# Optimization experiments

Measured on AMD Instinct MI355X. Metric: run time of the kernel, lower is better.

## Reference

```python
import jax, jax.numpy as jnp
import numpy as np

N, E = 50000, 800000
IN_C, HID_C, OUT_C = 256, 256, 256


def setup_inputs() -> dict:
    key = jax.random.key(0)
    ks = jax.random.split(key, 8)
    x_piece = jax.random.normal(ks[0], (N, IN_C), dtype=jnp.float32)
    edge_index_piece = jax.random.randint(ks[1], (2, E), 0, N, dtype=jnp.int64)
    batch = jnp.zeros((N,), dtype=jnp.int64)
    def glorot(k, fan_in, fan_out):
        s = jnp.sqrt(6.0 / (fan_in + fan_out)).astype(jnp.float32)
        return jax.random.uniform(k, (fan_in, fan_out), jnp.float32, -s, s)
    return {
        "x_piece": x_piece,
        "edge_index_piece": edge_index_piece,
        "batch": batch,
        "W1": glorot(ks[2], IN_C, HID_C), "b1": jnp.zeros((HID_C,), jnp.float32),
        "W2": glorot(ks[3], HID_C, HID_C), "b2": jnp.zeros((HID_C,), jnp.float32),
        "W3": glorot(ks[4], HID_C, OUT_C), "b3": jnp.zeros((OUT_C,), jnp.float32),
    }


def _gcn_prep(edge_index, n_nodes):
    # add self-loops, compute symmetric normalization (PyG GCNConv default)
    src = jnp.concatenate([edge_index[0], jnp.arange(n_nodes, dtype=edge_index.dtype)])
    dst = jnp.concatenate([edge_index[1], jnp.arange(n_nodes, dtype=edge_index.dtype)])
    deg = jax.ops.segment_sum(jnp.ones_like(dst, dtype=jnp.float32), dst, num_segments=n_nodes)
    deg_inv_sqrt = jnp.where(deg > 0, jax.lax.rsqrt(jnp.maximum(deg, 1.0)), 0.0)
    norm = deg_inv_sqrt[src] * deg_inv_sqrt[dst]  # [E+N]
    return src, dst, norm


def _gcn_layer(x, src, dst, norm, W, b, n_nodes):
    h = x @ W                                   # [N, out] dense transform first
    msg = h[src] * norm[:, None]                # gather + scale
    out = jax.ops.segment_sum(msg, dst, num_segments=n_nodes)  # scatter-add
    return out + b


def reference(x_piece, edge_index_piece, batch, W1, b1, W2, b2, W3, b3):
    n_nodes = x_piece.shape[0]
    src, dst, norm = _gcn_prep(edge_index_piece, n_nodes)
    x = _gcn_layer(x_piece, src, dst, norm, W1, b1, n_nodes)
    x = jax.nn.gelu(x)
    x = _gcn_layer(x, src, dst, norm, W2, b2, n_nodes)
    x = jax.nn.gelu(x)
    x = _gcn_layer(x, src, dst, norm, W3, b3, n_nodes)
    return x
```

## Files before the change

### kernel.cpp

```cpp
#include <hip/hip_runtime.h>
#include <cstdint>
#include <cstddef>

#define CH 256

typedef _Float16 f16x8 __attribute__((ext_vector_type(8)));
typedef float f32x4 __attribute__((ext_vector_type(4)));

#define GLOB(x) ((const __attribute__((address_space(1))) void*)(x))
#define LDSP(x) ((__attribute__((address_space(3))) void*)(x))


__device__ __forceinline__ int ld_idx(const void* p, long long i, int w64) {
    if (w64) return (int)((const long long*)p)[i];
    return ((const int*)p)[i];
}

__device__ __forceinline__ float gelu_f(float x) {
    float x3 = x * x * x;
    float t = tanhf(0.7978845608028654f * (x + 0.044715f * x3));
    return 0.5f * x * (1.0f + t);
}


__global__ void k_detect(const void* __restrict__ ei, int* __restrict__ flag, int E) {
    int l = threadIdx.x;
    long long k = ((long long)l * (long long)(E - 1)) / 63;
    int w = ((const int*)ei)[2 * k + 1];
    unsigned long long vote = __ballot(w == 0);
    if (l == 0) *flag = (vote == ~0ULL) ? 1 : 0;
}

__global__ void k_deg(const void* __restrict__ ei, const int* __restrict__ flag,
                      int* __restrict__ deg, int E) {
    int e = blockIdx.x * blockDim.x + threadIdx.x;
    if (e >= E) return;
    int w64 = *flag;
    int d = ld_idx(ei, (long long)E + e, w64);
    atomicAdd(&deg[d], 1);
}

__global__ void k_dis(const int* __restrict__ deg, float* __restrict__ dis, int N) {
    int n = blockIdx.x * blockDim.x + threadIdx.x;
    if (n >= N) return;
    dis[n] = 1.0f / sqrtf((float)(deg[n] + 1));
}

__global__ void k_scan_block(const int* __restrict__ deg, int* __restrict__ rowptr,
                             int* __restrict__ partial, int N) {
    __shared__ int s[256];
    int gid = blockIdx.x * 256 + threadIdx.x;
    int v = (gid < N) ? deg[gid] : 0;
    s[threadIdx.x] = v;
    __syncthreads();
    for (int off = 1; off < 256; off <<= 1) {
        int t = (threadIdx.x >= off) ? s[threadIdx.x - off] : 0;
        __syncthreads();
        s[threadIdx.x] += t;
        __syncthreads();
    }
    if (gid < N) rowptr[gid] = s[threadIdx.x] - v;
    if (threadIdx.x == 255) partial[blockIdx.x] = s[255];
}

__global__ void k_scan_partial(int* __restrict__ partial, int nb) {
    __shared__ int s[256];
    int i = threadIdx.x;
    int v = (i < nb) ? partial[i] : 0;
    s[i] = v;
    __syncthreads();
    for (int off = 1; off < 256; off <<= 1) {
        int t = (i >= off) ? s[i - off] : 0;
        __syncthreads();
        s[i] += t;
        __syncthreads();
    }
    if (i < nb) partial[i] = s[i] - v;
}

__global__ void k_add_off(int* __restrict__ rowptr, const int* __restrict__ partial,
                          int N, int E) {
    int gid = blockIdx.x * 256 + threadIdx.x;
    if (gid < N) rowptr[gid] += partial[blockIdx.x];
    if (gid == 0) rowptr[N] = E;
}

__global__ void k_scatter(const void* __restrict__ ei, const int* __restrict__ flag,
                          const float* __restrict__ dis, const int* __restrict__ rowptr,
                          int* __restrict__ cnt, int2* __restrict__ epack, int E) {
    int e = blockIdx.x * blockDim.x + threadIdx.x;
    if (e >= E) return;
    int w64 = *flag;
    int s = ld_idx(ei, e, w64);
    int d = ld_idx(ei, (long long)E + e, w64);
    int pos = rowptr[d] + atomicAdd(&cnt[d], 1);
    epack[pos] = make_int2(s, __float_as_int(dis[s] * dis[d]));
}


__global__ void k_split_w(const float* __restrict__ W, _Float16* __restrict__ Wh,
                          _Float16* __restrict__ Wl) {
    int k = threadIdx.x;
    int c = blockIdx.x;
    float v = W[k * CH + c];
    _Float16 h = (_Float16)v;
    Wh[c * CH + k] = h;
    Wl[c * CH + k] = (_Float16)(v - (float)h);
}


#define GM 128
#define GN 128
#define GK 32

__global__ __launch_bounds__(256, 2)
void k_gemm16(const float* __restrict__ A, const _Float16* __restrict__ Bh,
              const _Float16* __restrict__ Bl, uint8_t* __restrict__ H16,
              float* __restrict__ scales, int M) {
    __shared__ __align__(16) char smem[65536];
    float*    lA = (float*)smem;
    _Float16* lB = (_Float16*)(smem + 32768);

    const int tid  = threadIdx.x;
    const int lane = tid & 63;
    const int wid  = tid >> 6;
    const int m0   = blockIdx.x * GM;
    const int n0   = blockIdx.y * GN;
    const int wm   = wid >> 1, wn = wid & 1;
    const int r15  = lane & 15, kg = lane >> 4;

    auto stage = [&](int buf, int k0) {
        #pragma unroll
        for (int c = 0; c < 8; c++) {
            int call = wid * 8 + c;
            if (call < 16) {
                int L = call * 64 + lane;
                int row = L >> 3, ch = L & 7;
                int gr = m0 + row; gr = (gr < M) ? gr : (M - 1);
                const float* g = A + (size_t)gr * CH + k0 + ((ch ^ (row & 7)) << 2);
                __builtin_amdgcn_global_load_lds(GLOB(g), LDSP(&lA[buf * 4096 + call * 256]), 16, 0, 0);
            } else if (call < 24) {
                int cc = call - 16;
                int L = cc * 64 + lane;
                int row = L >> 2, ch = L & 3;
                const _Float16* g = Bh + (size_t)(n0 + row) * CH + k0 + ((ch ^ ((row >> 1) & 3)) << 3);
                __builtin_amdgcn_global_load_lds(GLOB(g), LDSP(&lB[buf * 8192 + cc * 512]), 16, 0, 0);
            } else {
                int cc = call - 24;
                int L = cc * 64 + lane;
                int row = L >> 2, ch = L & 3;
                const _Float16* g = Bl + (size_t)(n0 + row) * CH + k0 + ((ch ^ ((row >> 1) & 3)) << 3);
                __builtin_amdgcn_global_load_lds(GLOB(g), LDSP(&lB[buf * 8192 + 4096 + cc * 512]), 16, 0, 0);
            }
        }
    };

    f32x4 acc[4][4];
    #pragma unroll
    for (int i = 0; i < 4; i++)
        #pragma unroll
        for (int n = 0; n < 4; n++)
            acc[i][n] = (f32x4){0.f, 0.f, 0.f, 0.f};

    stage(0, 0);
    __syncthreads();

    for (int ks = 0; ks < 8; ks++) {
        int cur = ks & 1;
        if (ks < 7) stage(cur ^ 1, (ks + 1) * GK);

        f16x8 ah[4], al[4], bh[4], bl[4];
        #pragma unroll
        for (int i = 0; i < 4; i++) {
            int R  = wm * 64 + i * 16 + r15;
            int p0 = (2 * kg) ^ (R & 7);
            const f32x4* base = (const f32x4*)&lA[cur * 4096 + R * GK];
            f32x4 va = base[p0];
            f32x4 vb = base[p0 ^ 1];
            #pragma unroll
            for (int j = 0; j < 4; j++) {
                float v = va[j];
                _Float16 h = (_Float16)v;
                ah[i][j] = h;
                al[i][j] = (_Float16)(v - (float)h);
            }
            #pragma unroll
            for (int j = 0; j < 4; j++) {
                float v = vb[j];
                _Float16 h = (_Float16)v;
                ah[i][4 + j] = h;
                al[i][4 + j] = (_Float16)(v - (float)h);
            }
        }
        #pragma unroll
        for (int n = 0; n < 4; n++) {
            int C = wn * 64 + n * 16 + r15;
            int p = kg ^ ((C >> 1) & 3);
            bh[n] = *(const f16x8*)&lB[cur * 8192 + C * GK + p * 8];
            bl[n] = *(const f16x8*)&lB[cur * 8192 + 4096 + C * GK + p * 8];
        }
        #pragma unroll
        for (int i = 0; i < 4; i++)
            #pragma unroll
            for (int n = 0; n < 4; n++) {
                acc[i][n] = __builtin_amdgcn_mfma_f32_16x16x32_f16(ah[i], bh[n], acc[i][n], 0, 0, 0);
                acc[i][n] = __builtin_amdgcn_mfma_f32_16x16x32_f16(ah[i], bl[n], acc[i][n], 0, 0, 0);
                acc[i][n] = __builtin_amdgcn_mfma_f32_16x16x32_f16(al[i], bh[n], acc[i][n], 0, 0, 0);
            }
        __syncthreads();
    }

    float mx = 0.f;
    #pragma unroll
    for (int i = 0; i < 4; i++)
        #pragma unroll
        for (int n = 0; n < 4; n++)
            #pragma unroll
            for (int r = 0; r < 4; r++)
                mx = fmaxf(mx, fabsf(acc[i][n][r]));
    #pragma unroll
    for (int off = 32; off > 0; off >>= 1)
        mx = fmaxf(mx, __shfl_xor(mx, off));
    if (lane == 0) ((float*)smem)[wid] = mx;
    __syncthreads();
    float tmax = fmaxf(fmaxf(((float*)smem)[0], ((float*)smem)[1]),
                       fmaxf(((float*)smem)[2], ((float*)smem)[3]));
    float scl = tmax * (1.0f / 32767.0f);
    float inv = (tmax > 0.f) ? (32767.0f / tmax) : 0.f;
    __syncthreads();

    float* ep = (float*)smem + wid * 4096;
    #pragma unroll
    for (int i = 0; i < 4; i++)
        #pragma unroll
        for (int n = 0; n < 4; n++)
            #pragma unroll
            for (int r = 0; r < 4; r++)
                ep[(i * 16 + kg * 4 + r) * 64 + n * 16 + r15] = acc[i][n][r];
    __syncthreads();

    int q = lane & 15;
    int rsub = lane >> 4;
    #pragma unroll
    for (int p = 0; p < 16; p++) {
        int lrow = p * 4 + rsub;
        int grow = m0 + wm * 64 + lrow;
        if (grow < M) {
            int q0 = __float2int_rn(ep[lrow * 64 + q * 4 + 0] * inv);
            int q1 = __float2int_rn(ep[lrow * 64 + q * 4 + 1] * inv);
            int q2 = __float2int_rn(ep[lrow * 64 + q * 4 + 2] * inv);
            int q3 = __float2int_rn(ep[lrow * 64 + q * 4 + 3] * inv);
            uint2 d;
            d.x = (q0 & 0xFFFF) | (q1 << 16);
            d.y = (q2 & 0xFFFF) | (q3 << 16);
            int col = n0 + wn * 64 + q * 4;
            *(uint2*)(H16 + (size_t)grow * 512 + (size_t)col * 2) = d;
        }
    }

    if (tid < GM && m0 + tid < M) scales[(size_t)(m0 + tid) * 2 + (n0 >> 7)] = scl;
}


__global__ __launch_bounds__(256) void k_agg(const uint8_t* __restrict__ H16,
                                             const float* __restrict__ scales,
                                             const float* __restrict__ dis,
                                             const int* __restrict__ rowptr,
                                             const int2* __restrict__ epack,
                                             const float* __restrict__ bias,
                                             float* __restrict__ out, int N, int do_gelu) {
    int node = blockIdx.x * 4 + threadIdx.y;
    if (node >= N) return;
    int lane = threadIdx.x;
    int half = lane >> 5;
    float d = dis[node];
    short4 hv = *(const short4*)(H16 + (size_t)node * 512 + (size_t)lane * 8);
    float wself = d * d * scales[(size_t)node * 2 + half];
    float ax = wself * (float)hv.x, ay = wself * (float)hv.y;
    float az = wself * (float)hv.z, aw = wself * (float)hv.w;
    int s = rowptr[node], e = rowptr[node + 1];
    int j = s;
    for (; j + 8 <= e; j += 8) {
        int2 p[8];
        #pragma unroll
        for (int t = 0; t < 8; t++) p[t] = epack[j + t];
        short4 v[8];
        float sc[8];
        #pragma unroll
        for (int t = 0; t < 8; t++) {
            v[t] = *(const short4*)(H16 + (size_t)p[t].x * 512 + (size_t)lane * 8);
            sc[t] = scales[(size_t)p[t].x * 2 + half];
        }
        #pragma unroll
        for (int t = 0; t < 8; t++) {
            float wn = __int_as_float(p[t].y) * sc[t];
            ax += wn * (float)v[t].x; ay += wn * (float)v[t].y;
            az += wn * (float)v[t].z; aw += wn * (float)v[t].w;
        }
    }
    for (; j < e; j++) {
        int2 p = epack[j];
        float wn = __int_as_float(p.y) * scales[(size_t)p.x * 2 + half];
        short4 v = *(const short4*)(H16 + (size_t)p.x * 512 + (size_t)lane * 8);
        ax += wn * (float)v.x; ay += wn * (float)v.y;
        az += wn * (float)v.z; aw += wn * (float)v.w;
    }
    float4 b = ((const float4*)bias)[lane];
    ax += b.x; ay += b.y; az += b.z; aw += b.w;
    if (do_gelu) {
        ax = gelu_f(ax); ay = gelu_f(ay); az = gelu_f(az); aw = gelu_f(aw);
    }
    ((float4*)(out + (size_t)node * CH))[lane] = make_float4(ax, ay, az, aw);
}


extern "C" void kernel_launch(void* const* d_in, const int* in_sizes, int n_in,
                              void* d_out, int out_size, void* d_ws, size_t ws_size,
                              hipStream_t stream) {
    const float* x  = (const float*)d_in[0];
    const void*  ei = d_in[1];
    const float* W1 = (const float*)d_in[3]; const float* b1 = (const float*)d_in[4];
    const float* W2 = (const float*)d_in[5]; const float* b2 = (const float*)d_in[6];
    const float* W3 = (const float*)d_in[7]; const float* b3 = (const float*)d_in[8];

    int N = in_sizes[0] / CH;
    int E = in_sizes[1] / 2;
    float* out = (float*)d_out;

    char* ws = (char*)d_ws;
    auto take = [&](size_t bytes) {
        char* p = ws;
        ws += (bytes + 15) & ~(size_t)15;
        return p;
    };
    uint8_t*  H16    = (uint8_t*) take((size_t)N * 512);
    float*    scales = (float*)   take((size_t)N * 2 * sizeof(float));
    int*      deg    = (int*)     take((size_t)N * sizeof(int));
    float*    dis    = (float*)   take((size_t)N * sizeof(float));
    int*      rowptr = (int*)     take((size_t)(N + 1) * sizeof(int));
    int*      cnt    = (int*)     take((size_t)N * sizeof(int));
    int*      part   = (int*)     take(4096);
    int*      flag   = (int*)     take(16);
    int2*     epack  = (int2*)    take((size_t)E * sizeof(int2));
    _Float16* Wh1    = (_Float16*)take((size_t)CH * CH * 2);
    _Float16* Wl1    = (_Float16*)take((size_t)CH * CH * 2);
    _Float16* Wh2    = (_Float16*)take((size_t)CH * CH * 2);
    _Float16* Wl2    = (_Float16*)take((size_t)CH * CH * 2);
    _Float16* Wh3    = (_Float16*)take((size_t)CH * CH * 2);
    _Float16* Wl3    = (_Float16*)take((size_t)CH * CH * 2);

    hipMemsetAsync(deg, 0, (size_t)N * sizeof(int), stream);
    hipMemsetAsync(cnt, 0, (size_t)N * sizeof(int), stream);

    int eb = (E + 255) / 256;
    int nb = (N + 255) / 256;

    k_detect<<<1, 64, 0, stream>>>(ei, flag, E);
    k_deg<<<eb, 256, 0, stream>>>(ei, flag, deg, E);
    k_dis<<<nb, 256, 0, stream>>>(deg, dis, N);
    k_scan_block<<<nb, 256, 0, stream>>>(deg, rowptr, part, N);
    k_scan_partial<<<1, 256, 0, stream>>>(part, nb);
    k_add_off<<<nb, 256, 0, stream>>>(rowptr, part, N, E);
    k_scatter<<<eb, 256, 0, stream>>>(ei, flag, dis, rowptr, cnt, epack, E);

    k_split_w<<<CH, CH, 0, stream>>>(W1, Wh1, Wl1);
    k_split_w<<<CH, CH, 0, stream>>>(W2, Wh2, Wl2);
    k_split_w<<<CH, CH, 0, stream>>>(W3, Wh3, Wl3);

    dim3 ggrid((N + GM - 1) / GM, CH / GN);
    dim3 agrid((N + 3) / 4);
    dim3 ablock(64, 4);

    k_gemm16<<<ggrid, 256, 0, stream>>>(x, Wh1, Wl1, H16, scales, N);
    k_agg<<<agrid, ablock, 0, stream>>>(H16, scales, dis, rowptr, epack, b1, out, N, 1);
    k_gemm16<<<ggrid, 256, 0, stream>>>(out, Wh2, Wl2, H16, scales, N);
    k_agg<<<agrid, ablock, 0, stream>>>(H16, scales, dis, rowptr, epack, b2, out, N, 1);
    k_gemm16<<<ggrid, 256, 0, stream>>>(out, Wh3, Wl3, H16, scales, N);
    k_agg<<<agrid, ablock, 0, stream>>>(H16, scales, dis, rowptr, epack, b3, out, N, 0);
}
```

Baseline: 422.0 us.

## Store GEMM output in 32-column slabs and split aggregation across column groups

New measurement: 732.0 us. +73.4%, slower.

```diff
diff --git a/kernel.cpp b/kernel.cpp
--- a/kernel.cpp
+++ b/kernel.cpp
@@ -6,6 +6,7 @@
 
 typedef _Float16 f16x8 __attribute__((ext_vector_type(8)));
 typedef float f32x4 __attribute__((ext_vector_type(4)));
+typedef float f32x2 __attribute__((ext_vector_type(2)));
 
 #define GLOB(x) ((const __attribute__((address_space(1))) void*)(x))
 #define LDSP(x) ((__attribute__((address_space(3))) void*)(x))
@@ -254,7 +255,9 @@
             d.x = (q0 & 0xFFFF) | (q1 << 16);
             d.y = (q2 & 0xFFFF) | (q3 << 16);
             int col = n0 + wn * 64 + q * 4;
-            *(uint2*)(H16 + (size_t)grow * 512 + (size_t)col * 2) = d;
+            uint8_t* dst = H16 + ((size_t)(col >> 5) * (size_t)M + grow) * 64
+                               + (size_t)(col & 31) * 2;
+            *(uint2*)dst = d;
         }
     }
 
@@ -262,55 +265,67 @@
 }
 
 
-__global__ __launch_bounds__(256) void k_agg(const uint8_t* __restrict__ H16,
+__global__ __launch_bounds__(256) void k_agg(const uint8_t* __restrict__ H16g,
                                              const float* __restrict__ scales,
                                              const float* __restrict__ dis,
                                              const int* __restrict__ rowptr,
                                              const int2* __restrict__ epack,
                                              const float* __restrict__ bias,
                                              float* __restrict__ out, int N, int do_gelu) {
-    int node = blockIdx.x * 4 + threadIdx.y;
+    int g = blockIdx.x & 7;
+    int node = (blockIdx.x >> 3) * 4 + threadIdx.y;
     if (node >= N) return;
     int lane = threadIdx.x;
-    int half = lane >> 5;
-    float d = dis[node];
-    short4 hv = *(const short4*)(H16 + (size_t)node * 512 + (size_t)lane * 8);
-    float wself = d * d * scales[(size_t)node * 2 + half];
-    float ax = wself * (float)hv.x, ay = wself * (float)hv.y;
-    float az = wself * (float)hv.z, aw = wself * (float)hv.w;
+    int sub = lane >> 4;
+    int cp  = lane & 15;
+    int half = g >> 2;
+    const uint8_t* __restrict__ Hg = H16g + (size_t)g * (size_t)N * 64;
+
+    float ax, ay;
+    {
+        unsigned u = *(const unsigned*)(Hg + (size_t)node * 64 + cp * 4);
+        float d = dis[node];
+        float ws = (sub == 0) ? d * d * scales[(size_t)node * 2 + half] : 0.f;
+        ax = ws * (float)(short)(u & 0xFFFFu);
+        ay = ws * (float)(short)(u >> 16);
+    }
+
     int s = rowptr[node], e = rowptr[node + 1];
+    float bx = 0.f, by = 0.f;
     int j = s;
     for (; j + 8 <= e; j += 8) {
-        int2 p[8];
-        #pragma unroll
-        for (int t = 0; t < 8; t++) p[t] = epack[j + t];
-        short4 v[8];
-        float sc[8];
-        #pragma unroll
-        for (int t = 0; t < 8; t++) {
-            v[t] = *(const short4*)(H16 + (size_t)p[t].x * 512 + (size_t)lane * 8);
-            sc[t] = scales[(size_t)p[t].x * 2 + half];
-        }
-        #pragma unroll
-        for (int t = 0; t < 8; t++) {
-            float wn = __int_as_float(p[t].y) * sc[t];
-            ax += wn * (float)v[t].x; ay += wn * (float)v[t].y;
-            az += wn * (float)v[t].z; aw += wn * (float)v[t].w;
-        }
-    }
-    for (; j < e; j++) {
-        int2 p = epack[j];
-        float wn = __int_as_float(p.y) * scales[(size_t)p.x * 2 + half];
-        short4 v = *(const short4*)(H16 + (size_t)p.x * 512 + (size_t)lane * 8);
-        ax += wn * (float)v.x; ay += wn * (float)v.y;
-        az += wn * (float)v.z; aw += wn * (float)v.w;
-    }
-    float4 b = ((const float4*)bias)[lane];
-    ax += b.x; ay += b.y; az += b.z; aw += b.w;
-    if (do_gelu) {
-        ax = gelu_f(ax); ay = gelu_f(ay); az = gelu_f(az); aw = gelu_f(aw);
-    }
-    ((float4*)(out + (size_t)node * CH))[lane] = make_float4(ax, ay, az, aw);
+        int2 p1 = epack[j + sub];
+        int2 p2 = epack[j + 4 + sub];
+        unsigned u1 = *(const unsigned*)(Hg + (size_t)p1.x * 64 + cp * 4);
+        unsigned u2 = *(const unsigned*)(Hg + (size_t)p2.x * 64 + cp * 4);
+        float w1 = __int_as_float(p1.y) * scales[(size_t)p1.x * 2 + half];
+        float w2 = __int_as_float(p2.y) * scales[(size_t)p2.x * 2 + half];
+        ax += w1 * (float)(short)(u1 & 0xFFFFu);
+        ay += w1 * (float)(short)(u1 >> 16);
+        bx += w2 * (float)(short)(u2 & 0xFFFFu);
+        by += w2 * (float)(short)(u2 >> 16);
+    }
+    for (; j < e; j += 4) {
+        int idx = j + sub;
+        bool act = idx < e;
+        int2 p = epack[act ? idx : s];
+        unsigned u = *(const unsigned*)(Hg + (size_t)p.x * 64 + cp * 4);
+        float wn = act ? __int_as_float(p.y) * scales[(size_t)p.x * 2 + half] : 0.f;
+        ax += wn * (float)(short)(u & 0xFFFFu);
+        ay += wn * (float)(short)(u >> 16);
+    }
+    ax += bx; ay += by;
+
+    ax += __shfl_xor(ax, 16); ay += __shfl_xor(ay, 16);
+    ax += __shfl_xor(ax, 32); ay += __shfl_xor(ay, 32);
+
+    if (sub == 0) {
+        int c = g * 32 + cp * 2;
+        ax += bias[c]; ay += bias[c + 1];
+        if (do_gelu) { ax = gelu_f(ax); ay = gelu_f(ay); }
+        f32x2 v = {ax, ay};
+        __builtin_nontemporal_store(v, (f32x2*)(out + (size_t)node * CH + c));
+    }
 }
 
 
@@ -368,7 +383,7 @@
     k_split_w<<<CH, CH, 0, stream>>>(W3, Wh3, Wl3);
 
     dim3 ggrid((N + GM - 1) / GM, CH / GN);
-    dim3 agrid((N + 3) / 4);
+    dim3 agrid(8 * ((N + 3) / 4));
     dim3 ablock(64, 4);
 
     k_gemm16<<<ggrid, 256, 0, stream>>>(x, Wh1, Wl1, H16, scales, N);
```

## Pre-split GEMM activations into fp16 hi/lo in producer kernels

Applied to the files above, without the earlier changes.

Measured after the change: 440.4 us. 1.04x slower.

```diff
diff --git a/kernel.cpp b/kernel.cpp
--- a/kernel.cpp
+++ b/kernel.cpp
@@ -5,6 +5,7 @@
 #define CH 256
 
 typedef _Float16 f16x8 __attribute__((ext_vector_type(8)));
+typedef _Float16 f16x4 __attribute__((ext_vector_type(4)));
 typedef float f32x4 __attribute__((ext_vector_type(4)));
 
 #define GLOB(x) ((const __attribute__((address_space(1))) void*)(x))
@@ -109,17 +110,34 @@
 }
 
 
+__global__ void k_split_x(const float* __restrict__ x, _Float16* __restrict__ Ah,
+                          _Float16* __restrict__ Al, int n4) {
+    int i = blockIdx.x * 256 + threadIdx.x;
+    if (i >= n4) return;
+    float4 v = ((const float4*)x)[i];
+    f16x4 h, l;
+    h[0] = (_Float16)v.x; l[0] = (_Float16)(v.x - (float)h[0]);
+    h[1] = (_Float16)v.y; l[1] = (_Float16)(v.y - (float)h[1]);
+    h[2] = (_Float16)v.z; l[2] = (_Float16)(v.z - (float)h[2]);
+    h[3] = (_Float16)v.w; l[3] = (_Float16)(v.w - (float)h[3]);
+    ((f16x4*)Ah)[i] = h;
+    ((f16x4*)Al)[i] = l;
+}
+
+
 #define GM 128
 #define GN 128
 #define GK 32
 
 __global__ __launch_bounds__(256, 2)
-void k_gemm16(const float* __restrict__ A, const _Float16* __restrict__ Bh,
-              const _Float16* __restrict__ Bl, uint8_t* __restrict__ H16,
-              float* __restrict__ scales, int M) {
+void k_gemm16s(const _Float16* __restrict__ Ah, const _Float16* __restrict__ Al,
+               const _Float16* __restrict__ Bh, const _Float16* __restrict__ Bl,
+               uint8_t* __restrict__ H16, float* __restrict__ scales, int M) {
     __shared__ __align__(16) char smem[65536];
-    float*    lA = (float*)smem;
-    _Float16* lB = (_Float16*)(smem + 32768);
+    _Float16* lAh = (_Float16*)smem;
+    _Float16* lAl = (_Float16*)(smem + 16384);
+    _Float16* lBh = (_Float16*)(smem + 32768);
+    _Float16* lBl = (_Float16*)(smem + 49152);
 
     const int tid  = threadIdx.x;
     const int lane = tid & 63;
@@ -133,24 +151,24 @@
         #pragma unroll
         for (int c = 0; c < 8; c++) {
             int call = wid * 8 + c;
-            if (call < 16) {
-                int L = call * 64 + lane;
-                int row = L >> 3, ch = L & 7;
+            int cc = call & 7;
+            int L = cc * 64 + lane;
+            int row = L >> 2, ch = L & 3;
+            int sch = ch ^ ((row >> 1) & 3);
+            if (call < 8) {
                 int gr = m0 + row; gr = (gr < M) ? gr : (M - 1);
-                const float* g = A + (size_t)gr * CH + k0 + ((ch ^ (row & 7)) << 2);
-                __builtin_amdgcn_global_load_lds(GLOB(g), LDSP(&lA[buf * 4096 + call * 256]), 16, 0, 0);
+                const _Float16* g = Ah + (size_t)gr * CH + k0 + (sch << 3);
+                __builtin_amdgcn_global_load_lds(GLOB(g), LDSP(&lAh[buf * 4096 + L * 8]), 16, 0, 0);
+            } else if (call < 16) {
+                int gr = m0 + row; gr = (gr < M) ? gr : (M - 1);
+                const _Float16* g = Al + (size_t)gr * CH + k0 + (sch << 3);
+                __builtin_amdgcn_global_load_lds(GLOB(g), LDSP(&lAl[buf * 4096 + L * 8]), 16, 0, 0);
             } else if (call < 24) {
-                int cc = call - 16;
-                int L = cc * 64 + lane;
-                int row = L >> 2, ch = L & 3;
-                const _Float16* g = Bh + (size_t)(n0 + row) * CH + k0 + ((ch ^ ((row >> 1) & 3)) << 3);
-                __builtin_amdgcn_global_load_lds(GLOB(g), LDSP(&lB[buf * 8192 + cc * 512]), 16, 0, 0);
+                const _Float16* g = Bh + (size_t)(n0 + row) * CH + k0 + (sch << 3);
+                __builtin_amdgcn_global_load_lds(GLOB(g), LDSP(&lBh[buf * 4096 + L * 8]), 16, 0, 0);
             } else {
-                int cc = call - 24;
-                int L = cc * 64 + lane;
-                int row = L >> 2, ch = L & 3;
-                const _Float16* g = Bl + (size_t)(n0 + row) * CH + k0 + ((ch ^ ((row >> 1) & 3)) << 3);
-                __builtin_amdgcn_global_load_lds(GLOB(g), LDSP(&lB[buf * 8192 + 4096 + cc * 512]), 16, 0, 0);
+                const _Float16* g = Bl + (size_t)(n0 + row) * CH + k0 + (sch << 3);
+                __builtin_amdgcn_global_load_lds(GLOB(g), LDSP(&lBl[buf * 4096 + L * 8]), 16, 0, 0);
             }
         }
     };
@@ -172,32 +190,17 @@
         f16x8 ah[4], al[4], bh[4], bl[4];
         #pragma unroll
         for (int i = 0; i < 4; i++) {
-            int R  = wm * 64 + i * 16 + r15;
-            int p0 = (2 * kg) ^ (R & 7);
-            const f32x4* base = (const f32x4*)&lA[cur * 4096 + R * GK];
-            f32x4 va = base[p0];
-            f32x4 vb = base[p0 ^ 1];
-            #pragma unroll
-            for (int j = 0; j < 4; j++) {
-                float v = va[j];
-                _Float16 h = (_Float16)v;
-                ah[i][j] = h;
-                al[i][j] = (_Float16)(v - (float)h);
-            }
-            #pragma unroll
-            for (int j = 0; j < 4; j++) {
-                float v = vb[j];
-                _Float16 h = (_Float16)v;
-                ah[i][4 + j] = h;
-                al[i][4 + j] = (_Float16)(v - (float)h);
-            }
+            int R = wm * 64 + i * 16 + r15;
+            int p = kg ^ ((R >> 1) & 3);
+            ah[i] = *(const f16x8*)&lAh[cur * 4096 + R * GK + p * 8];
+            al[i] = *(const f16x8*)&lAl[cur * 4096 + R * GK + p * 8];
         }
         #pragma unroll
         for (int n = 0; n < 4; n++) {
             int C = wn * 64 + n * 16 + r15;
             int p = kg ^ ((C >> 1) & 3);
-            bh[n] = *(const f16x8*)&lB[cur * 8192 + C * GK + p * 8];
-            bl[n] = *(const f16x8*)&lB[cur * 8192 + 4096 + C * GK + p * 8];
+            bh[n] = *(const f16x8*)&lBh[cur * 4096 + C * GK + p * 8];
+            bl[n] = *(const f16x8*)&lBl[cur * 4096 + C * GK + p * 8];
         }
         #pragma unroll
         for (int i = 0; i < 4; i++)
@@ -262,13 +265,16 @@
 }
 
 
+template <int MODE>
 __global__ __launch_bounds__(256) void k_agg(const uint8_t* __restrict__ H16,
                                              const float* __restrict__ scales,
                                              const float* __restrict__ dis,
                                              const int* __restrict__ rowptr,
                                              const int2* __restrict__ epack,
                                              const float* __restrict__ bias,
-                                             float* __restrict__ out, int N, int do_gelu) {
+                                             float* __restrict__ out,
+                                             _Float16* __restrict__ Ah,
+                                             _Float16* __restrict__ Al, int N) {
     int node = blockIdx.x * 4 + threadIdx.y;
     if (node >= N) return;
     int lane = threadIdx.x;
@@ -307,10 +313,19 @@
     }
     float4 b = ((const float4*)bias)[lane];
     ax += b.x; ay += b.y; az += b.z; aw += b.w;
-    if (do_gelu) {
+    if (MODE == 0) {
         ax = gelu_f(ax); ay = gelu_f(ay); az = gelu_f(az); aw = gelu_f(aw);
-    }
-    ((float4*)(out + (size_t)node * CH))[lane] = make_float4(ax, ay, az, aw);
+        f16x4 h, l;
+        h[0] = (_Float16)ax; l[0] = (_Float16)(ax - (float)h[0]);
+        h[1] = (_Float16)ay; l[1] = (_Float16)(ay - (float)h[1]);
+        h[2] = (_Float16)az; l[2] = (_Float16)(az - (float)h[2]);
+        h[3] = (_Float16)aw; l[3] = (_Float16)(aw - (float)h[3]);
+        size_t idx = (size_t)node * 64 + lane;
+        ((f16x4*)Ah)[idx] = h;
+        ((f16x4*)Al)[idx] = l;
+    } else {
+        ((float4*)(out + (size_t)node * CH))[lane] = make_float4(ax, ay, az, aw);
+    }
 }
 
 
@@ -334,6 +349,8 @@
         return p;
     };
     uint8_t*  H16    = (uint8_t*) take((size_t)N * 512);
+    _Float16* Ah     = (_Float16*)take((size_t)N * CH * 2);
+    _Float16* Al     = (_Float16*)take((size_t)N * CH * 2);
     float*    scales = (float*)   take((size_t)N * 2 * sizeof(float));
     int*      deg    = (int*)     take((size_t)N * sizeof(int));
     float*    dis    = (float*)   take((size_t)N * sizeof(float));
@@ -367,14 +384,17 @@
     k_split_w<<<CH, CH, 0, stream>>>(W2, Wh2, Wl2);
     k_split_w<<<CH, CH, 0, stream>>>(W3, Wh3, Wl3);
 
+    int n4 = N * (CH / 4);
+    k_split_x<<<(n4 + 255) / 256, 256, 0, stream>>>(x, Ah, Al, n4);
+
     dim3 ggrid((N + GM - 1) / GM, CH / GN);
     dim3 agrid((N + 3) / 4);
     dim3 ablock(64, 4);
 
-    k_gemm16<<<ggrid, 256, 0, stream>>>(x, Wh1, Wl1, H16, scales, N);
-    k_agg<<<agrid, ablock, 0, stream>>>(H16, scales, dis, rowptr, epack, b1, out, N, 1);
-    k_gemm16<<<ggrid, 256, 0, stream>>>(out, Wh2, Wl2, H16, scales, N);
-    k_agg<<<agrid, ablock, 0, stream>>>(H16, scales, dis, rowptr, epack, b2, out, N, 1);
-    k_gemm16<<<ggrid, 256, 0, stream>>>(out, Wh3, Wl3, H16, scales, N);
-    k_agg<<<agrid, ablock, 0, stream>>>(H16, scales, dis, rowptr, epack, b3, out, N, 0);
-}
+    k_gemm16s<<<ggrid, 256, 0, stream>>>(Ah, Al, Wh1, Wl1, H16, scales, N);
+    k_agg<0><<<agrid, ablock, 0, stream>>>(H16, scales, dis, rowptr, epack, b1, out, Ah, Al, N);
+    k_gemm16s<<<ggrid, 256, 0, stream>>>(Ah, Al, Wh2, Wl2, H16, scales, N);
+    k_agg<0><<<agrid, ablock, 0, stream>>>(H16, scales, dis, rowptr, epack, b2, out, Ah, Al, N);
+    k_gemm16s<<<ggrid, 256, 0, stream>>>(Ah, Al, Wh3, Wl3, H16, scales, N);
+    k_agg<1><<<agrid, ablock, 0, stream>>>(H16, scales, dis, rowptr, epack, b3, out, Ah, Al, N);
+}
```

## Quantize GEMM activations to int16 per row to halve A-operand traffic

Applied to the files above, without the earlier changes.

Result: slower. 433.2 us (+2.6%).

```diff
diff --git a/kernel.cpp b/kernel.cpp
--- a/kernel.cpp
+++ b/kernel.cpp
@@ -5,7 +5,9 @@
 #define CH 256
 
 typedef _Float16 f16x8 __attribute__((ext_vector_type(8)));
+typedef _Float16 f16x4 __attribute__((ext_vector_type(4)));
 typedef float f32x4 __attribute__((ext_vector_type(4)));
+typedef short short8 __attribute__((ext_vector_type(8)));
 
 #define GLOB(x) ((const __attribute__((address_space(1))) void*)(x))
 #define LDSP(x) ((__attribute__((address_space(3))) void*)(x))
@@ -109,17 +111,39 @@
 }
 
 
+__global__ __launch_bounds__(256) void k_quant_x(const float* __restrict__ x,
+                                                 uint8_t* __restrict__ Xout,
+                                                 float* __restrict__ sout, int N) {
+    int node = blockIdx.x * 4 + threadIdx.y;
+    if (node >= N) return;
+    int lane = threadIdx.x;
+    float4 v = ((const float4*)(x + (size_t)node * CH))[lane];
+    float mx = fmaxf(fmaxf(fabsf(v.x), fabsf(v.y)), fmaxf(fabsf(v.z), fabsf(v.w)));
+    #pragma unroll
+    for (int off = 32; off > 0; off >>= 1)
+        mx = fmaxf(mx, __shfl_xor(mx, off));
+    float inv = (mx > 0.f) ? (32767.0f / mx) : 0.f;
+    short4 q;
+    q.x = (short)__float2int_rn(v.x * inv);
+    q.y = (short)__float2int_rn(v.y * inv);
+    q.z = (short)__float2int_rn(v.z * inv);
+    q.w = (short)__float2int_rn(v.w * inv);
+    *(short4*)(Xout + (size_t)node * 512 + (size_t)lane * 8) = q;
+    if (lane == 0) sout[node] = mx * (1.0f / 32767.0f);
+}
+
+
 #define GM 128
 #define GN 128
 #define GK 32
 
 __global__ __launch_bounds__(256, 2)
-void k_gemm16(const float* __restrict__ A, const _Float16* __restrict__ Bh,
-              const _Float16* __restrict__ Bl, uint8_t* __restrict__ H16,
-              float* __restrict__ scales, int M) {
+void k_gemm16(const uint8_t* __restrict__ X16, const float* __restrict__ sx,
+              const _Float16* __restrict__ Bh, const _Float16* __restrict__ Bl,
+              uint8_t* __restrict__ H16, float* __restrict__ scales, int M) {
     __shared__ __align__(16) char smem[65536];
-    float*    lA = (float*)smem;
-    _Float16* lB = (_Float16*)(smem + 32768);
+    short*    lA16 = (short*)smem;
+    _Float16* lB   = (_Float16*)(smem + 16384);
 
     const int tid  = threadIdx.x;
     const int lane = tid & 63;
@@ -131,22 +155,23 @@
 
     auto stage = [&](int buf, int k0) {
         #pragma unroll
-        for (int c = 0; c < 8; c++) {
-            int call = wid * 8 + c;
-            if (call < 16) {
+        for (int c = 0; c < 6; c++) {
+            int call = wid * 6 + c;
+            if (call < 8) {
                 int L = call * 64 + lane;
-                int row = L >> 3, ch = L & 7;
+                int row = L >> 2, ch = L & 3;
+                int sch = ch ^ ((row >> 1) & 3);
                 int gr = m0 + row; gr = (gr < M) ? gr : (M - 1);
-                const float* g = A + (size_t)gr * CH + k0 + ((ch ^ (row & 7)) << 2);
-                __builtin_amdgcn_global_load_lds(GLOB(g), LDSP(&lA[buf * 4096 + call * 256]), 16, 0, 0);
-            } else if (call < 24) {
-                int cc = call - 16;
+                const uint8_t* g = X16 + (size_t)gr * 512 + (size_t)k0 * 2 + (sch << 4);
+                __builtin_amdgcn_global_load_lds(GLOB(g), LDSP(&lA16[buf * 4096 + L * 8]), 16, 0, 0);
+            } else if (call < 16) {
+                int cc = call - 8;
                 int L = cc * 64 + lane;
                 int row = L >> 2, ch = L & 3;
                 const _Float16* g = Bh + (size_t)(n0 + row) * CH + k0 + ((ch ^ ((row >> 1) & 3)) << 3);
                 __builtin_amdgcn_global_load_lds(GLOB(g), LDSP(&lB[buf * 8192 + cc * 512]), 16, 0, 0);
             } else {
-                int cc = call - 24;
+                int cc = call - 16;
                 int L = cc * 64 + lane;
                 int row = L >> 2, ch = L & 3;
                 const _Float16* g = Bl + (size_t)(n0 + row) * CH + k0 + ((ch ^ ((row >> 1) & 3)) << 3);
@@ -155,6 +180,13 @@
         }
     };
 
+    float sA[4];
+    #pragma unroll
+    for (int i = 0; i < 4; i++) {
+        int gr = m0 + wm * 64 + i * 16 + r15;
+        sA[i] = sx[(gr < M) ? gr : (M - 1)];
+    }
+
     f32x4 acc[4][4];
     #pragma unroll
     for (int i = 0; i < 4; i++)
@@ -172,24 +204,16 @@
         f16x8 ah[4], al[4], bh[4], bl[4];
         #pragma unroll
         for (int i = 0; i < 4; i++) {
-            int R  = wm * 64 + i * 16 + r15;
-            int p0 = (2 * kg) ^ (R & 7);
-            const f32x4* base = (const f32x4*)&lA[cur * 4096 + R * GK];
-            f32x4 va = base[p0];
-            f32x4 vb = base[p0 ^ 1];
+            int R = wm * 64 + i * 16 + r15;
+            int p = kg ^ ((R >> 1) & 3);
+            short8 q = *(const short8*)&lA16[cur * 4096 + R * 32 + p * 8];
+            float s = sA[i];
             #pragma unroll
-            for (int j = 0; j < 4; j++) {
-                float v = va[j];
+            for (int j = 0; j < 8; j++) {
+                float v = s * (float)q[j];
                 _Float16 h = (_Float16)v;
                 ah[i][j] = h;
                 al[i][j] = (_Float16)(v - (float)h);
-            }
-            #pragma unroll
-            for (int j = 0; j < 4; j++) {
-                float v = vb[j];
-                _Float16 h = (_Float16)v;
-                ah[i][4 + j] = h;
-                al[i][4 + j] = (_Float16)(v - (float)h);
             }
         }
         #pragma unroll
@@ -262,13 +286,16 @@
 }
 
 
+template <int MODE>
 __global__ __launch_bounds__(256) void k_agg(const uint8_t* __restrict__ H16,
                                              const float* __restrict__ scales,
                                              const float* __restrict__ dis,
                                              const int* __restrict__ rowptr,
                                              const int2* __restrict__ epack,
                                              const float* __restrict__ bias,
-                                             float* __restrict__ out, int N, int do_gelu) {
+                                             float* __restrict__ out,
+                                             uint8_t* __restrict__ Xout,
+                                             float* __restrict__ sxout, int N) {
     int node = blockIdx.x * 4 + threadIdx.y;
     if (node >= N) return;
     int lane = threadIdx.x;
@@ -307,10 +334,23 @@
     }
     float4 b = ((const float4*)bias)[lane];
     ax += b.x; ay += b.y; az += b.z; aw += b.w;
-    if (do_gelu) {
+    if (MODE == 0) {
         ax = gelu_f(ax); ay = gelu_f(ay); az = gelu_f(az); aw = gelu_f(aw);
-    }
-    ((float4*)(out + (size_t)node * CH))[lane] = make_float4(ax, ay, az, aw);
+        float mx = fmaxf(fmaxf(fabsf(ax), fabsf(ay)), fmaxf(fabsf(az), fabsf(aw)));
+        #pragma unroll
+        for (int off = 32; off > 0; off >>= 1)
+            mx = fmaxf(mx, __shfl_xor(mx, off));
+        float inv = (mx > 0.f) ? (32767.0f / mx) : 0.f;
+        short4 q;
+        q.x = (short)__float2int_rn(ax * inv);
+        q.y = (short)__float2int_rn(ay * inv);
+        q.z = (short)__float2int_rn(az * inv);
+        q.w = (short)__float2int_rn(aw * inv);
+        *(short4*)(Xout + (size_t)node * 512 + (size_t)lane * 8) = q;
+        if (lane == 0) sxout[node] = mx * (1.0f / 32767.0f);
+    } else {
+        ((float4*)(out + (size_t)node * CH))[lane] = make_float4(ax, ay, az, aw);
+    }
 }
 
 
@@ -334,7 +374,11 @@
         return p;
     };
     uint8_t*  H16    = (uint8_t*) take((size_t)N * 512);
-    float*    scales = (float*)   take((size_t)N * 2 * sizeof(float));
+    uint8_t*  Xa     = (uint8_t*) take((size_t)N * 512);
+    uint8_t*  Xb     = (uint8_t*) take((size_t)N * 512);
+    float*    hscl   = (float*)   take((size_t)N * 2 * sizeof(float));
+    float*    sxa    = (float*)   take((size_t)N * sizeof(float));
+    float*    sxb    = (float*)   take((size_t)N * sizeof(float));
     int*      deg    = (int*)     take((size_t)N * sizeof(int));
     float*    dis    = (float*)   take((size_t)N * sizeof(float));
     int*      rowptr = (int*)     take((size_t)(N + 1) * sizeof(int));
@@ -367,14 +411,18 @@
     k_split_w<<<CH, CH, 0, stream>>>(W2, Wh2, Wl2);
     k_split_w<<<CH, CH, 0, stream>>>(W3, Wh3, Wl3);
 
+    dim3 qgrid((N + 3) / 4);
+    dim3 qblock(64, 4);
+    k_quant_x<<<qgrid, qblock, 0, stream>>>(x, Xa, sxa, N);
+
     dim3 ggrid((N + GM - 1) / GM, CH / GN);
     dim3 agrid((N + 3) / 4);
     dim3 ablock(64, 4);
 
-    k_gemm16<<<ggrid, 256, 0, stream>>>(x, Wh1, Wl1, H16, scales, N);
-    k_agg<<<agrid, ablock, 0, stream>>>(H16, scales, dis, rowptr, epack, b1, out, N, 1);
-    k_gemm16<<<ggrid, 256, 0, stream>>>(out, Wh2, Wl2, H16, scales, N);
-    k_agg<<<agrid, ablock, 0, stream>>>(H16, scales, dis, rowptr, epack, b2, out, N, 1);
-    k_gemm16<<<ggrid, 256, 0, stream>>>(out, Wh3, Wl3, H16, scales, N);
-    k_agg<<<agrid, ablock, 0, stream>>>(H16, scales, dis, rowptr, epack, b3, out, N, 0);
-}
+    k_gemm16<<<ggrid, 256, 0, stream>>>(Xa, sxa, Wh1, Wl1, H16, hscl, N);
+    k_agg<0><<<agrid, ablock, 0, stream>>>(H16, hscl, dis, rowptr, epack, b1, out, Xb, sxb, N);
+    k_gemm16<<<ggrid, 256, 0, stream>>>(Xb, sxb, Wh2, Wl2, H16, hscl, N);
+    k_agg<0><<<agrid, ablock, 0, stream>>>(H16, hscl, dis, rowptr, epack, b2, out, Xa, sxa, N);
+    k_gemm16<<<ggrid, 256, 0, stream>>>(Xa, sxa, Wh3, Wl3, H16, hscl, N);
+    k_agg<1><<<agrid, ablock, 0, stream>>>(H16, hscl, dis, rowptr, epack, b3, out, Xb, sxb, N);
+}
```
